# Kernel optimization log

Measured on AMD Instinct MI355X. Metric: run time of the kernel, lower is better.

The kernel has to match this reference:

```python
import jax, jax.numpy as jnp
import numpy as np

DIST = 45
HID = 128
NLAYERS = 4
BATCH = 128


def _build_edges(d):
    n = d * d - 1
    sqrt_n = int(np.sqrt(n)) + 1
    src, dst = [], []
    for i in range(n):
        row, col = i // sqrt_n, i % sqrt_n
        for dr, dc in ((-1, 0), (1, 0), (0, -1), (0, 1)):
            nr, nc = row + dr, col + dc
            j = nr * sqrt_n + nc
            if 0 <= nr < sqrt_n and 0 <= j < n and j != i:
                src.append(i)
                dst.append(j)
    return np.asarray(src, np.int32), np.asarray(dst, np.int32), n


def setup_inputs() -> dict:
    key = jax.random.key(0)
    ks = jax.random.split(key, 8)
    src, dst, n = _build_edges(DIST)
    s = 1.0 / np.sqrt(HID)
    return {
        "x": jax.random.normal(ks[0], (BATCH, n), jnp.float32),
        "W_embed": jax.random.normal(ks[1], (1, HID), jnp.float32),
        "b_embed": jnp.zeros((HID,), jnp.float32),
        "gnn_W": jax.random.normal(ks[2], (NLAYERS, 2 * HID, HID), jnp.float32) * s,
        "gnn_b": jnp.zeros((NLAYERS, HID), jnp.float32),
        "ln_g": jnp.ones((NLAYERS, HID), jnp.float32),
        "ln_b": jnp.zeros((NLAYERS, HID), jnp.float32),
        "out_W1": jax.random.normal(ks[3], (HID, HID), jnp.float32) * s,
        "out_b1": jnp.zeros((HID,), jnp.float32),
        "out_W2": jax.random.normal(ks[4], (HID, 2), jnp.float32) * s,
        "out_b2": jnp.zeros((2,), jnp.float32),
        "edge_src": jnp.asarray(src),
        "edge_dst": jnp.asarray(dst),
    }


def _layer_norm(h, g, b, eps=1e-5):
    mu = h.mean(-1, keepdims=True)
    var = ((h - mu) ** 2).mean(-1, keepdims=True)
    return (h - mu) * jax.lax.rsqrt(var + eps) * g + b


def _segment_mean(h, src, dst, n_nodes):
    # h: [B, N, H] -> mean of incoming-neighbor features per node; 0 if no edge.
    hs = jnp.swapaxes(h[:, src, :], 0, 1)                 # [E, B, H]
    sums = jax.ops.segment_sum(hs, dst, num_segments=n_nodes)   # [N, B, H]
    cnt = jax.ops.segment_sum(jnp.ones_like(dst, jnp.float32), dst,
                              num_segments=n_nodes)              # [N]
    agg = jnp.where(cnt[:, None, None] > 0,
                    sums / jnp.maximum(cnt, 1.0)[:, None, None], 0.0)
    return jnp.swapaxes(agg, 0, 1)                        # [B, N, H]


def reference(x, W_embed, b_embed, gnn_W, gnn_b, ln_g, ln_b,
              out_W1, out_b1, out_W2, out_b2, edge_src, edge_dst):
    n_nodes = x.shape[1]
    # node_embed: Linear(1, H) applied to x[..., None]
    h = x[..., None] * W_embed[0] + b_embed               # [B, N, H]
    for l in range(gnn_W.shape[0]):
        agg = _segment_mean(h, edge_src, edge_dst, n_nodes)
        combined = jnp.concatenate([h, agg], axis=-1)     # [B, N, 2H]
        h = jax.nn.relu(combined @ gnn_W[l] + gnn_b[l])
        h = _layer_norm(h, ln_g[l], ln_b[l])
    graph_repr = h.mean(axis=1)                           # [B, H]
    hid = jax.nn.relu(graph_repr @ out_W1 + out_b1)
    return hid @ out_W2 + out_b2                          # [B, 2]
```

## Files before the change

### kernel.cpp

```cpp
#include <hip/hip_runtime.h>

typedef unsigned short u16;
typedef unsigned int   u32;
typedef __attribute__((ext_vector_type(8))) short short8;
typedef __attribute__((ext_vector_type(4))) float f32x4;

#define NN   2024
#define NB   128
#define HID  128
#define MT   128
#define MTOT (NN*NB)

__device__ __forceinline__ float bf2f(u16 h){ union{u32 u; float f;}c; c.u=((u32)h)<<16; return c.f; }
__device__ __forceinline__ u16 f2bf(float f){ union{float f; u32 u;}c; c.f=f; return (u16)((c.u+0x7fffu+((c.u>>16)&1u))>>16); }
__device__ __forceinline__ f32x4 mfma16(short8 a, short8 b, f32x4 c){ return __builtin_amdgcn_mfma_f32_16x16x32_bf16(a,b,c,0,0,0); }
__device__ __forceinline__ void glds16(const void* g, void* l){
  __builtin_amdgcn_global_load_lds((const __attribute__((address_space(1))) void*)g,
                                   (__attribute__((address_space(3))) void*)l, 16, 0, 0);
}

__device__ __forceinline__ void gemm_chunk(f32x4 (&acc)[2][4], const u16* Ab,
                                           const u16* Wb, int l, int wr, int wc){
  const u32 swz   = ((u32)(l & 7)) << 4;
  const u32 klane = ((u32)(l >> 4)) << 4;
  const char* aB = (const char*)Ab + (u32)(32*wr + (l & 15)) * 256;
  const char* bB = (const char*)Wb + (u32)(64*wc + (l & 15)) * 256;
#pragma unroll
  for (int ks = 0; ks < 4; ++ks){
    const u32 kbx = (((u32)ks << 6) + klane) ^ swz;
    short8 a0 = *(const short8*)(aB + kbx);
    short8 a1 = *(const short8*)(aB + 4096 + kbx);
#pragma unroll
    for (int j = 0; j < 4; ++j){
      short8 bf = *(const short8*)(bB + (u32)j*4096 + kbx);
      acc[0][j] = mfma16(a0, bf, acc[0][j]);
      acc[1][j] = mfma16(a1, bf, acc[1][j]);
    }
  }
}

template<int EMBED>
__global__ __launch_bounds__(512, 4)
void layer_k(const u16* __restrict__ hin, const float* __restrict__ x,
             const float* __restrict__ We, const float* __restrict__ be,
             const u16* __restrict__ Wt, const float* __restrict__ bias,
             const float* __restrict__ lng, const float* __restrict__ lnb,
             u16* __restrict__ hout)
{
  __shared__ __align__(16) u16 Ab[MT*128];
  __shared__ __align__(16) u16 Wb[128*128];
  const int t  = threadIdx.x;
  const int l  = t & 63;
  const int wv = t >> 6;
  const int wr = wv >> 1;
  const int wc = wv & 1;
  const int m0 = blockIdx.x * MT;

  const int gl16 = l >> 4, gcl = l & 15;

  const int sR = t >> 2;
  const int cq = t & 3;
  const int c0 = cq * 4;
  const int sm = m0 + sR;
  const u32 sSwz = ((u32)(sR & 7)) << 4;
  char* aRow = (char*)Ab + (u32)sR * 256;

  const int nd = sm % NN;
  const int v0 = (nd >= 45), v1 = (nd <= NN-46), v2 = (nd >= 1), v3 = (nd <= NN-2);
  const float inv = 1.0f / (float)(v0 + v1 + v2 + v3);

  f32x4 acc[2][4];
#pragma unroll
  for (int m = 0; m < 2; ++m)
#pragma unroll
    for (int j = 0; j < 4; ++j)
      acc[m][j] = (f32x4){0.f,0.f,0.f,0.f};

  if constexpr (EMBED) {
    const float xv = x[sm];
#pragma unroll
    for (int q = 0; q < 4; ++q){
      const int c = c0 + q;
      short8 v;
#pragma unroll
      for (int i = 0; i < 8; ++i) v[i] = (short)f2bf(fmaf(xv, We[c*8+i], be[c*8+i]));
      *(short8*)(aRow + (((u32)c << 4) ^ sSwz)) = v;
    }
  } else {
#pragma unroll
    for (int i = 0; i < 4; ++i){
      const int r  = wv*16 + i*4 + gl16;
      const int cs = gcl ^ (r & 7);
      glds16(hin + (size_t)(m0 + r)*HID + cs*8, (char*)Ab + (u32)(wv*4 + i)*1024);
    }
  }
#pragma unroll
  for (int i = 0; i < 4; ++i){
    const int col = wv*16 + i*4 + gl16;
    const int cs  = gcl ^ (col & 7);
    glds16(Wt + (u32)col*256 + cs*8, (char*)Wb + (u32)(wv*4 + i)*1024);
  }

  short8 gA[4], gB[4];
  if constexpr (!EMBED) {
    const u16* p0 = hin + (size_t)(v0 ? sm-45 : sm) * HID;
    const u16* p1 = hin + (size_t)(v1 ? sm+45 : sm) * HID;
#pragma unroll
    for (int q = 0; q < 4; ++q){
      gA[q] = *(const short8*)(p0 + (c0+q)*8);
      gB[q] = *(const short8*)(p1 + (c0+q)*8);
    }
  }
  __syncthreads();

  gemm_chunk(acc, Ab, Wb, l, wr, wc);

  float sq[4][8];
  short8 gC[4], gD[4];
  float mx = 0.f;
  if constexpr (!EMBED) {
    const u16* p2 = hin + (size_t)(v2 ? sm-1 : sm) * HID;
    const u16* p3 = hin + (size_t)(v3 ? sm+1 : sm) * HID;
#pragma unroll
    for (int q = 0; q < 4; ++q){
      gC[q] = *(const short8*)(p2 + (c0+q)*8);
      gD[q] = *(const short8*)(p3 + (c0+q)*8);
    }
    const float f0 = (float)v0, f1 = (float)v1;
#pragma unroll
    for (int q = 0; q < 4; ++q)
#pragma unroll
      for (int i = 0; i < 8; ++i)
        sq[q][i] = f0*bf2f((u16)gA[q][i]) + f1*bf2f((u16)gB[q][i]);
  } else {
    if (v0) mx += x[sm-45];
    if (v1) mx += x[sm+45];
    if (v2) mx += x[sm-1];
    if (v3) mx += x[sm+1];
    mx *= inv;
  }
  __syncthreads();

  if constexpr (!EMBED) {
    const float f2 = (float)v2, f3 = (float)v3;
#pragma unroll
    for (int q = 0; q < 4; ++q){
      short8 v;
#pragma unroll
      for (int i = 0; i < 8; ++i){
        const float s = (sq[q][i] + f2*bf2f((u16)gC[q][i]) + f3*bf2f((u16)gD[q][i])) * inv;
        v[i] = (short)f2bf(s);
      }
      *(short8*)(aRow + (((u32)(c0+q) << 4) ^ sSwz)) = v;
    }
  } else {
#pragma unroll
    for (int q = 0; q < 4; ++q){
      const int c = c0 + q;
      short8 v;
#pragma unroll
      for (int i = 0; i < 8; ++i) v[i] = (short)f2bf(fmaf(mx, We[c*8+i], be[c*8+i]));
      *(short8*)(aRow + (((u32)c << 4) ^ sSwz)) = v;
    }
  }
#pragma unroll
  for (int i = 0; i < 4; ++i){
    const int col = wv*16 + i*4 + gl16;
    const int cs  = gcl ^ (col & 7);
    glds16(Wt + (u32)col*256 + 128 + cs*8, (char*)Wb + (u32)(wv*4 + i)*1024);
  }
  __syncthreads();

  gemm_chunk(acc, Ab, Wb, l, wr, wc);
  __syncthreads();

  float2* red = (float2*)Ab;
  const int cB = l & 15, rg = l >> 4;
  float bias4[4], g4[4], be4[4];
#pragma unroll
  for (int j = 0; j < 4; ++j){
    const int col = 64*wc + 16*j + cB;
    bias4[j] = bias[col]; g4[j] = lng[col]; be4[j] = lnb[col];
  }
#pragma unroll
  for (int m = 0; m < 2; ++m){
#pragma unroll
    for (int r = 0; r < 4; ++r){
      float p1 = 0.f, p2 = 0.f;
#pragma unroll
      for (int j = 0; j < 4; ++j){
        float y = fmaxf(acc[m][j][r] + bias4[j], 0.f);
        acc[m][j][r] = y;
        p1 += y; p2 += y*y;
      }
#pragma unroll
      for (int d = 1; d < 16; d <<= 1){
        p1 += __shfl_xor(p1, d);
        p2 += __shfl_xor(p2, d);
      }
      if (cB == 0){
        const int row = 32*wr + 16*m + 4*rg + r;
        red[row*2 + wc] = make_float2(p1, p2);
      }
    }
  }
  __syncthreads();
#pragma unroll
  for (int m = 0; m < 2; ++m){
#pragma unroll
    for (int r = 0; r < 4; ++r){
      const int row = 32*wr + 16*m + 4*rg + r;
      const float2 pa = red[row*2], pb = red[row*2 + 1];
      const float s1 = pa.x + pb.x, s2 = pa.y + pb.y;
      const float mu  = s1 * (1.f/128.f);
      const float var = s2 * (1.f/128.f) - mu*mu;
      const float rs  = rsqrtf(var + 1e-5f);
      u16* orow = hout + (size_t)(m0 + row) * HID;
#pragma unroll
      for (int j = 0; j < 4; ++j){
        const float o = (acc[m][j][r] - mu) * rs * g4[j] + be4[j];
        orow[64*wc + 16*j + cB] = f2bf(o);
      }
    }
  }
}

__global__ void prep_k(const float* __restrict__ gw, u16* __restrict__ Wt){
  const int idx = blockIdx.x*256 + threadIdx.x;
  const int lay = idx >> 15;
  const int r   = idx & 32767;
  const int j   = r >> 8;
  const int k   = r & 255;
  Wt[idx] = f2bf(gw[lay*32768 + k*128 + j]);
}

__global__ void mean1_k(const u16* __restrict__ h, float* __restrict__ partial){
  __shared__ float red[16][16][8];
  const int blk = blockIdx.x;
  const int b = blk >> 3, s = blk & 7;
  const int t = threadIdx.x;
  const int cg = t & 15, q = t >> 4;
  const int nbeg = s*253, nend = nbeg + 253;
  float a[8] = {0.f,0.f,0.f,0.f,0.f,0.f,0.f,0.f};
  const u16* hb = h + (size_t)b * NN * HID;
  for (int n = nbeg + q; n < nend; n += 16){
    short8 v = *(const short8*)(hb + (size_t)n*HID + cg*8);
#pragma unroll
    for (int i = 0; i < 8; ++i) a[i] += bf2f((u16)v[i]);
  }
#pragma unroll
  for (int i = 0; i < 8; ++i) red[q][cg][i] = a[i];
  __syncthreads();
  if (t < 128){
    const int cc = t >> 3, i = t & 7;
    float v = 0.f;
#pragma unroll
    for (int qq = 0; qq < 16; ++qq) v += red[qq][cc][i];
    partial[((size_t)b*8 + s)*128 + t] = v;
  }
}

__global__ void mean2_k(const float* __restrict__ partial, float* __restrict__ gr){
  const int idx = blockIdx.x*256 + threadIdx.x;
  const int b = idx >> 7, c = idx & 127;
  float a = 0.f;
#pragma unroll
  for (int s = 0; s < 8; ++s) a += partial[((size_t)b*8 + s)*128 + c];
  gr[idx] = a * (1.0f / 2024.0f);
}

__global__ void head1_k(const float* __restrict__ gr, const float* __restrict__ W1,
                        const float* __restrict__ b1, float* __restrict__ hid){
  const int idx = blockIdx.x*256 + threadIdx.x;
  const int b = idx >> 7, j = idx & 127;
  const float* g = gr + b*128;
  float a = b1[j];
  for (int k = 0; k < 128; ++k) a = fmaf(g[k], W1[k*128 + j], a);
  hid[idx] = fmaxf(a, 0.f);
}

__global__ void head2_k(const float* __restrict__ hid, const float* __restrict__ W2,
                        const float* __restrict__ b2, float* __restrict__ out){
  const int t = threadIdx.x;
  const int b = t >> 1, o = t & 1;
  const float* hh = hid + b*128;
  float a = b2[o];
  for (int k = 0; k < 128; ++k) a = fmaf(hh[k], W2[k*2 + o], a);
  out[t] = a;
}

extern "C" void kernel_launch(void* const* d_in, const int* in_sizes, int n_in,
                              void* d_out, int out_size, void* d_ws, size_t ws_size,
                              hipStream_t stream){
  const float* x  = (const float*)d_in[0];
  const float* We = (const float*)d_in[1];
  const float* be = (const float*)d_in[2];
  const float* gW = (const float*)d_in[3];
  const float* gb = (const float*)d_in[4];
  const float* lg = (const float*)d_in[5];
  const float* lb = (const float*)d_in[6];
  const float* W1 = (const float*)d_in[7];
  const float* b1 = (const float*)d_in[8];
  const float* W2 = (const float*)d_in[9];
  const float* b2 = (const float*)d_in[10];
  float* out = (float*)d_out;

  char* w = (char*)d_ws;
  const size_t HB = (size_t)MTOT * HID * 2;
  u16*   hA  = (u16*)w;
  u16*   hB  = (u16*)(w + HB);
  u16*   Wt  = (u16*)(w + 2*HB);
  float* gr  = (float*)(w + 2*HB + 262144);
  float* hid = (float*)(w + 2*HB + 262144 + 65536);
  float* partial = (float*)w;

  prep_k<<<512, 256, 0, stream>>>(gW, Wt);
  layer_k<1><<<MTOT/MT, 512, 0, stream>>>(nullptr, x, We, be, Wt,
                                          gb, lg, lb, hA);
  layer_k<0><<<MTOT/MT, 512, 0, stream>>>(hA, nullptr, nullptr, nullptr, Wt + 32768,
                                          gb + 128, lg + 128, lb + 128, hB);
  layer_k<0><<<MTOT/MT, 512, 0, stream>>>(hB, nullptr, nullptr, nullptr, Wt + 65536,
                                          gb + 256, lg + 256, lb + 256, hA);
  layer_k<0><<<MTOT/MT, 512, 0, stream>>>(hA, nullptr, nullptr, nullptr, Wt + 98304,
                                          gb + 384, lg + 384, lb + 384, hB);
  mean1_k<<<NB*8, 256, 0, stream>>>(hB, partial);
  mean2_k<<<64, 256, 0, stream>>>(partial, gr);
  head1_k<<<64, 256, 0, stream>>>(gr, W1, b1, hid);
  head2_k<<<1, 256, 0, stream>>>(hid, W2, b2, out);
}
```

Before: 309.3 us.

## Rewrite GNN layer kernel to feed MFMA operands directly from global memory

Rewrites the layer kernel so that weights and node features are loaded straight from global memory into registers as MFMA operands, using a transposed (W × H) orientation, instead of staging them through LDS with global_load_lds. Each block now covers 256 rows, and block IDs are remapped to XCD-contiguous chunks to improve L2 locality. Neighbour averaging is done in registers with precomputed weights and packed bf16 conversion. The output is transposed through LDS so global stores are coalesced. The trade-off is less on-chip reuse of weights and neighbour rows, since each wave now reads redundant data from L2, plus higher register pressure from the 4x4 accumulator tile.

```diff
diff --git a/kernel.cpp b/kernel.cpp
--- a/kernel.cpp
+++ b/kernel.cpp
@@ -8,220 +8,211 @@
 #define NN   2024
 #define NB   128
 #define HID  128
-#define MT   128
 #define MTOT (NN*NB)
-
+#define RPB  256
+#define NBLK (MTOT/RPB)
+
+__device__ __forceinline__ float bflo(u32 w){ union{u32 u; float f;}c; c.u=w<<16;        return c.f; }
+__device__ __forceinline__ float bfhi(u32 w){ union{u32 u; float f;}c; c.u=w&0xffff0000u; return c.f; }
 __device__ __forceinline__ float bf2f(u16 h){ union{u32 u; float f;}c; c.u=((u32)h)<<16; return c.f; }
 __device__ __forceinline__ u16 f2bf(float f){ union{float f; u32 u;}c; c.f=f; return (u16)((c.u+0x7fffu+((c.u>>16)&1u))>>16); }
-__device__ __forceinline__ f32x4 mfma16(short8 a, short8 b, f32x4 c){ return __builtin_amdgcn_mfma_f32_16x16x32_bf16(a,b,c,0,0,0); }
-__device__ __forceinline__ void glds16(const void* g, void* l){
-  __builtin_amdgcn_global_load_lds((const __attribute__((address_space(1))) void*)g,
-                                   (__attribute__((address_space(3))) void*)l, 16, 0, 0);
-}
-
-__device__ __forceinline__ void gemm_chunk(f32x4 (&acc)[2][4], const u16* Ab,
-                                           const u16* Wb, int l, int wr, int wc){
-  const u32 swz   = ((u32)(l & 7)) << 4;
-  const u32 klane = ((u32)(l >> 4)) << 4;
-  const char* aB = (const char*)Ab + (u32)(32*wr + (l & 15)) * 256;
-  const char* bB = (const char*)Wb + (u32)(64*wc + (l & 15)) * 256;
-#pragma unroll
-  for (int ks = 0; ks < 4; ++ks){
-    const u32 kbx = (((u32)ks << 6) + klane) ^ swz;
-    short8 a0 = *(const short8*)(aB + kbx);
-    short8 a1 = *(const short8*)(aB + 4096 + kbx);
-#pragma unroll
-    for (int j = 0; j < 4; ++j){
-      short8 bf = *(const short8*)(bB + (u32)j*4096 + kbx);
-      acc[0][j] = mfma16(a0, bf, acc[0][j]);
-      acc[1][j] = mfma16(a1, bf, acc[1][j]);
-    }
-  }
+__device__ __forceinline__ u32 cvtpk(float lo, float hi){
+  u32 r; asm("v_cvt_pk_bf16_f32 %0, %1, %2" : "=v"(r) : "v"(lo), "v"(hi)); return r;
+}
+__device__ __forceinline__ f32x4 mfma16(short8 a, short8 b, f32x4 c){
+  return __builtin_amdgcn_mfma_f32_16x16x32_bf16(a,b,c,0,0,0);
+}
+
+__device__ __forceinline__ short8 avg4(short8 a0, short8 a1, short8 a2, short8 a3,
+                                       float w0, float w1, float w2, float w3){
+  union{short8 s; u32 u[4];} A, B, C, D, R;
+  A.s=a0; B.s=a1; C.s=a2; D.s=a3;
+#pragma unroll
+  for (int p=0;p<4;++p){
+    float lo = w0*bflo(A.u[p]); lo = fmaf(w1,bflo(B.u[p]),lo); lo = fmaf(w2,bflo(C.u[p]),lo); lo = fmaf(w3,bflo(D.u[p]),lo);
+    float hi = w0*bfhi(A.u[p]); hi = fmaf(w1,bfhi(B.u[p]),hi); hi = fmaf(w2,bfhi(C.u[p]),hi); hi = fmaf(w3,bfhi(D.u[p]),hi);
+    R.u[p] = cvtpk(lo, hi);
+  }
+  return R.s;
+}
+
+__device__ __forceinline__ short8 synth8(float xv, const float* __restrict__ Wek,
+                                         const float* __restrict__ bek){
+  union{short8 s; u32 u[4];} R;
+#pragma unroll
+  for (int p=0;p<4;++p){
+    float lo = fmaf(xv, Wek[2*p],   bek[2*p]);
+    float hi = fmaf(xv, Wek[2*p+1], bek[2*p+1]);
+    R.u[p] = cvtpk(lo, hi);
+  }
+  return R.s;
 }
 
 template<int EMBED>
 __global__ __launch_bounds__(512, 4)
-void layer_k(const u16* __restrict__ hin, const float* __restrict__ x,
-             const float* __restrict__ We, const float* __restrict__ be,
-             const u16* __restrict__ Wt, const float* __restrict__ bias,
-             const float* __restrict__ lng, const float* __restrict__ lnb,
-             u16* __restrict__ hout)
+void layer2_k(const u16* __restrict__ hin, const float* __restrict__ x,
+              const float* __restrict__ We, const float* __restrict__ be,
+              const u16* __restrict__ Wt, const float* __restrict__ bias,
+              const float* __restrict__ lng, const float* __restrict__ lnb,
+              u16* __restrict__ hout)
 {
-  __shared__ __align__(16) u16 Ab[MT*128];
-  __shared__ __align__(16) u16 Wb[128*128];
+  __shared__ __align__(16) u16 trBuf[RPB*128];
   const int t  = threadIdx.x;
   const int l  = t & 63;
-  const int wv = t >> 6;
-  const int wr = wv >> 1;
-  const int wc = wv & 1;
-  const int m0 = blockIdx.x * MT;
-
-  const int gl16 = l >> 4, gcl = l & 15;
-
-  const int sR = t >> 2;
-  const int cq = t & 3;
-  const int c0 = cq * 4;
-  const int sm = m0 + sR;
-  const u32 sSwz = ((u32)(sR & 7)) << 4;
-  char* aRow = (char*)Ab + (u32)sR * 256;
-
-  const int nd = sm % NN;
-  const int v0 = (nd >= 45), v1 = (nd <= NN-46), v2 = (nd >= 1), v3 = (nd <= NN-2);
-  const float inv = 1.0f / (float)(v0 + v1 + v2 + v3);
-
-  f32x4 acc[2][4];
-#pragma unroll
-  for (int m = 0; m < 2; ++m)
-#pragma unroll
-    for (int j = 0; j < 4; ++j)
-      acc[m][j] = (f32x4){0.f,0.f,0.f,0.f};
-
-  if constexpr (EMBED) {
-    const float xv = x[sm];
-#pragma unroll
-    for (int q = 0; q < 4; ++q){
-      const int c = c0 + q;
-      short8 v;
-#pragma unroll
-      for (int i = 0; i < 8; ++i) v[i] = (short)f2bf(fmaf(xv, We[c*8+i], be[c*8+i]));
-      *(short8*)(aRow + (((u32)c << 4) ^ sSwz)) = v;
-    }
-  } else {
-#pragma unroll
-    for (int i = 0; i < 4; ++i){
-      const int r  = wv*16 + i*4 + gl16;
-      const int cs = gcl ^ (r & 7);
-      glds16(hin + (size_t)(m0 + r)*HID + cs*8, (char*)Ab + (u32)(wv*4 + i)*1024);
-    }
-  }
-#pragma unroll
-  for (int i = 0; i < 4; ++i){
-    const int col = wv*16 + i*4 + gl16;
-    const int cs  = gcl ^ (col & 7);
-    glds16(Wt + (u32)col*256 + cs*8, (char*)Wb + (u32)(wv*4 + i)*1024);
-  }
-
-  short8 gA[4], gB[4];
-  if constexpr (!EMBED) {
-    const u16* p0 = hin + (size_t)(v0 ? sm-45 : sm) * HID;
-    const u16* p1 = hin + (size_t)(v1 ? sm+45 : sm) * HID;
-#pragma unroll
-    for (int q = 0; q < 4; ++q){
-      gA[q] = *(const short8*)(p0 + (c0+q)*8);
-      gB[q] = *(const short8*)(p1 + (c0+q)*8);
+  const int wv = t >> 6, wr = wv >> 1, wc = wv & 1;
+  const int cB = l & 15, rg = l >> 4;
+
+  const int orig = blockIdx.x;
+  const int xcd = orig & 7, bidx = orig >> 3;
+  const int swzb = (xcd < 4 ? xcd*127 : 508 + (xcd-4)*126) + bidx;
+  const int m0 = swzb * RPB;
+  const int rowb = m0 + 64*wr;
+
+  int   rowi[4], r0[4], r1[4], r2[4], r3[4];
+  float fw0[4], fw1[4], fw2[4], fw3[4];
+  float xs[4], mx[4];
+#pragma unroll
+  for (int hm=0; hm<4; ++hm){
+    const int row = rowb + 16*hm + cB;
+    rowi[hm] = row;
+    const int nd = row % NN;
+    const int v0 = (nd >= 45), v1 = (nd <= NN-46), v2 = (nd >= 1), v3 = (nd <= NN-2);
+    const int cnt = v0+v1+v2+v3;
+    const float inv = (cnt==4) ? 0.25f : ((cnt==3) ? (1.f/3.f) : 0.5f);
+    fw0[hm] = v0 ? inv : 0.f; fw1[hm] = v1 ? inv : 0.f;
+    fw2[hm] = v2 ? inv : 0.f; fw3[hm] = v3 ? inv : 0.f;
+    r0[hm] = v0 ? row-45 : row; r1[hm] = v1 ? row+45 : row;
+    r2[hm] = v2 ? row-1  : row; r3[hm] = v3 ? row+1  : row;
+    if constexpr (EMBED){
+      xs[hm] = x[row];
+      mx[hm] = fw0[hm]*x[r0[hm]] + fw1[hm]*x[r1[hm]] + fw2[hm]*x[r2[hm]] + fw3[hm]*x[r3[hm]];
+    }
+  }
+
+  f32x4 acc[4][4];
+#pragma unroll
+  for (int fj=0; fj<4; ++fj)
+#pragma unroll
+    for (int hm=0; hm<4; ++hm)
+      acc[fj][hm] = (f32x4){0.f,0.f,0.f,0.f};
+
+  const int kb = rg*8;
+
+#pragma unroll
+  for (int ks=0; ks<4; ++ks){
+    const int kk = ks*32 + kb;
+    short8 aW[4];
+#pragma unroll
+    for (int fj=0; fj<4; ++fj){
+      const int feat = 64*wc + 16*fj + cB;
+      aW[fj] = *(const short8*)(Wt + (u32)feat*256 + kk);
+    }
+#pragma unroll
+    for (int hm=0; hm<4; ++hm){
+      short8 bH;
+      if constexpr (EMBED) bH = synth8(xs[hm], We+kk, be+kk);
+      else                 bH = *(const short8*)(hin + (size_t)rowi[hm]*HID + kk);
+#pragma unroll
+      for (int fj=0; fj<4; ++fj) acc[fj][hm] = mfma16(aW[fj], bH, acc[fj][hm]);
+    }
+  }
+#pragma unroll
+  for (int ks=0; ks<4; ++ks){
+    const int kk = ks*32 + kb;
+    short8 aW[4];
+#pragma unroll
+    for (int fj=0; fj<4; ++fj){
+      const int feat = 64*wc + 16*fj + cB;
+      aW[fj] = *(const short8*)(Wt + (u32)feat*256 + 128 + kk);
+    }
+#pragma unroll
+    for (int hm=0; hm<4; ++hm){
+      short8 bH;
+      if constexpr (EMBED) bH = synth8(mx[hm], We+kk, be+kk);
+      else {
+        short8 n0 = *(const short8*)(hin + (size_t)r0[hm]*HID + kk);
+        short8 n1 = *(const short8*)(hin + (size_t)r1[hm]*HID + kk);
+        short8 n2 = *(const short8*)(hin + (size_t)r2[hm]*HID + kk);
+        short8 n3 = *(const short8*)(hin + (size_t)r3[hm]*HID + kk);
+        bH = avg4(n0,n1,n2,n3, fw0[hm],fw1[hm],fw2[hm],fw3[hm]);
+      }
+#pragma unroll
+      for (int fj=0; fj<4; ++fj) acc[fj][hm] = mfma16(aW[fj], bH, acc[fj][hm]);
+    }
+  }
+
+  float4 bias4[4], g4[4], b4[4];
+#pragma unroll
+  for (int fj=0; fj<4; ++fj){
+    const int f0 = 64*wc + 16*fj + 4*rg;
+    bias4[fj] = *(const float4*)(bias + f0);
+    g4[fj]    = *(const float4*)(lng  + f0);
+    b4[fj]    = *(const float4*)(lnb  + f0);
+  }
+  float2* red = (float2*)trBuf;
+
+#pragma unroll
+  for (int hm=0; hm<4; ++hm){
+    float s1 = 0.f, s2 = 0.f;
+#pragma unroll
+    for (int fj=0; fj<4; ++fj){
+#pragma unroll
+      for (int rr=0; rr<4; ++rr){
+        const float bb = (rr==0)?bias4[fj].x:(rr==1)?bias4[fj].y:(rr==2)?bias4[fj].z:bias4[fj].w;
+        float y = fmaxf(acc[fj][hm][rr] + bb, 0.f);
+        acc[fj][hm][rr] = y;
+        s1 += y; s2 += y*y;
+      }
+    }
+    s1 += __shfl_xor(s1,16); s1 += __shfl_xor(s1,32);
+    s2 += __shfl_xor(s2,16); s2 += __shfl_xor(s2,32);
+    if (rg == 0){
+      const int rib = 64*wr + 16*hm + cB;
+      red[rib*2 + wc] = make_float2(s1, s2);
     }
   }
   __syncthreads();
 
-  gemm_chunk(acc, Ab, Wb, l, wr, wc);
-
-  float sq[4][8];
-  short8 gC[4], gD[4];
-  float mx = 0.f;
-  if constexpr (!EMBED) {
-    const u16* p2 = hin + (size_t)(v2 ? sm-1 : sm) * HID;
-    const u16* p3 = hin + (size_t)(v3 ? sm+1 : sm) * HID;
-#pragma unroll
-    for (int q = 0; q < 4; ++q){
-      gC[q] = *(const short8*)(p2 + (c0+q)*8);
-      gD[q] = *(const short8*)(p3 + (c0+q)*8);
-    }
-    const float f0 = (float)v0, f1 = (float)v1;
-#pragma unroll
-    for (int q = 0; q < 4; ++q)
-#pragma unroll
-      for (int i = 0; i < 8; ++i)
-        sq[q][i] = f0*bf2f((u16)gA[q][i]) + f1*bf2f((u16)gB[q][i]);
-  } else {
-    if (v0) mx += x[sm-45];
-    if (v1) mx += x[sm+45];
-    if (v2) mx += x[sm-1];
-    if (v3) mx += x[sm+1];
-    mx *= inv;
+  float mu4[4], rs4[4];
+#pragma unroll
+  for (int hm=0; hm<4; ++hm){
+    const int rib = 64*wr + 16*hm + cB;
+    const float2 A = red[rib*2], B = red[rib*2+1];
+    const float s1 = A.x + B.x, s2 = A.y + B.y;
+    const float mu  = s1 * (1.f/128.f);
+    const float var = s2 * (1.f/128.f) - mu*mu;
+    mu4[hm] = mu;
+    rs4[hm] = rsqrtf(var + 1e-5f);
   }
   __syncthreads();
 
-  if constexpr (!EMBED) {
-    const float f2 = (float)v2, f3 = (float)v3;
-#pragma unroll
-    for (int q = 0; q < 4; ++q){
-      short8 v;
-#pragma unroll
-      for (int i = 0; i < 8; ++i){
-        const float s = (sq[q][i] + f2*bf2f((u16)gC[q][i]) + f3*bf2f((u16)gD[q][i])) * inv;
-        v[i] = (short)f2bf(s);
-      }
-      *(short8*)(aRow + (((u32)(c0+q) << 4) ^ sSwz)) = v;
-    }
-  } else {
-#pragma unroll
-    for (int q = 0; q < 4; ++q){
-      const int c = c0 + q;
-      short8 v;
-#pragma unroll
-      for (int i = 0; i < 8; ++i) v[i] = (short)f2bf(fmaf(mx, We[c*8+i], be[c*8+i]));
-      *(short8*)(aRow + (((u32)c << 4) ^ sSwz)) = v;
-    }
-  }
-#pragma unroll
-  for (int i = 0; i < 4; ++i){
-    const int col = wv*16 + i*4 + gl16;
-    const int cs  = gcl ^ (col & 7);
-    glds16(Wt + (u32)col*256 + 128 + cs*8, (char*)Wb + (u32)(wv*4 + i)*1024);
+#pragma unroll
+  for (int hm=0; hm<4; ++hm){
+    const int rib = 64*wr + 16*hm + cB;
+    const u32 sw = ((u32)(rib & 7)) << 4;
+    char* rowp = (char*)trBuf + (u32)rib*256;
+    const float mu = mu4[hm], rs = rs4[hm];
+#pragma unroll
+    for (int fj=0; fj<4; ++fj){
+      const float y0 = fmaf((acc[fj][hm][0]-mu)*rs, g4[fj].x, b4[fj].x);
+      const float y1 = fmaf((acc[fj][hm][1]-mu)*rs, g4[fj].y, b4[fj].y);
+      const float y2 = fmaf((acc[fj][hm][2]-mu)*rs, g4[fj].z, b4[fj].z);
+      const float y3 = fmaf((acc[fj][hm][3]-mu)*rs, g4[fj].w, b4[fj].w);
+      const u32 off = (u32)(128*wc + 32*fj + 8*rg);
+      *(u32*)(rowp + ((off    ) ^ sw)) = cvtpk(y0, y1);
+      *(u32*)(rowp + ((off + 4) ^ sw)) = cvtpk(y2, y3);
+    }
   }
   __syncthreads();
 
-  gemm_chunk(acc, Ab, Wb, l, wr, wc);
-  __syncthreads();
-
-  float2* red = (float2*)Ab;
-  const int cB = l & 15, rg = l >> 4;
-  float bias4[4], g4[4], be4[4];
-#pragma unroll
-  for (int j = 0; j < 4; ++j){
-    const int col = 64*wc + 16*j + cB;
-    bias4[j] = bias[col]; g4[j] = lng[col]; be4[j] = lnb[col];
-  }
-#pragma unroll
-  for (int m = 0; m < 2; ++m){
-#pragma unroll
-    for (int r = 0; r < 4; ++r){
-      float p1 = 0.f, p2 = 0.f;
-#pragma unroll
-      for (int j = 0; j < 4; ++j){
-        float y = fmaxf(acc[m][j][r] + bias4[j], 0.f);
-        acc[m][j][r] = y;
-        p1 += y; p2 += y*y;
-      }
-#pragma unroll
-      for (int d = 1; d < 16; d <<= 1){
-        p1 += __shfl_xor(p1, d);
-        p2 += __shfl_xor(p2, d);
-      }
-      if (cB == 0){
-        const int row = 32*wr + 16*m + 4*rg + r;
-        red[row*2 + wc] = make_float2(p1, p2);
-      }
-    }
-  }
-  __syncthreads();
-#pragma unroll
-  for (int m = 0; m < 2; ++m){
-#pragma unroll
-    for (int r = 0; r < 4; ++r){
-      const int row = 32*wr + 16*m + 4*rg + r;
-      const float2 pa = red[row*2], pb = red[row*2 + 1];
-      const float s1 = pa.x + pb.x, s2 = pa.y + pb.y;
-      const float mu  = s1 * (1.f/128.f);
-      const float var = s2 * (1.f/128.f) - mu*mu;
-      const float rs  = rsqrtf(var + 1e-5f);
-      u16* orow = hout + (size_t)(m0 + row) * HID;
-#pragma unroll
-      for (int j = 0; j < 4; ++j){
-        const float o = (acc[m][j][r] - mu) * rs * g4[j] + be4[j];
-        orow[64*wc + 16*j + cB] = f2bf(o);
-      }
-    }
+  const int orow = t >> 1, half = t & 1;
+  const u32 sw2 = ((u32)(orow & 7)) << 4;
+  u16* dst = hout + (size_t)(m0 + orow)*HID + half*64;
+  const char* srow = (const char*)trBuf + (u32)orow*256;
+#pragma unroll
+  for (int i=0; i<8; ++i){
+    short8 v = *(const short8*)(srow + (((u32)(half*128 + 16*i)) ^ sw2));
+    *(short8*)(dst + i*8) = v;
   }
 }
 
@@ -315,14 +306,14 @@
   float* partial = (float*)w;
 
   prep_k<<<512, 256, 0, stream>>>(gW, Wt);
-  layer_k<1><<<MTOT/MT, 512, 0, stream>>>(nullptr, x, We, be, Wt,
-                                          gb, lg, lb, hA);
-  layer_k<0><<<MTOT/MT, 512, 0, stream>>>(hA, nullptr, nullptr, nullptr, Wt + 32768,
-                                          gb + 128, lg + 128, lb + 128, hB);
-  layer_k<0><<<MTOT/MT, 512, 0, stream>>>(hB, nullptr, nullptr, nullptr, Wt + 65536,
-                                          gb + 256, lg + 256, lb + 256, hA);
-  layer_k<0><<<MTOT/MT, 512, 0, stream>>>(hA, nullptr, nullptr, nullptr, Wt + 98304,
-                                          gb + 384, lg + 384, lb + 384, hB);
+  layer2_k<1><<<NBLK, 512, 0, stream>>>(nullptr, x, We, be, Wt,
+                                        gb, lg, lb, hA);
+  layer2_k<0><<<NBLK, 512, 0, stream>>>(hA, nullptr, nullptr, nullptr, Wt + 32768,
+                                        gb + 128, lg + 128, lb + 128, hB);
+  layer2_k<0><<<NBLK, 512, 0, stream>>>(hB, nullptr, nullptr, nullptr, Wt + 65536,
+                                        gb + 256, lg + 256, lb + 256, hA);
+  layer2_k<0><<<NBLK, 512, 0, stream>>>(hA, nullptr, nullptr, nullptr, Wt + 98304,
+                                        gb + 384, lg + 384, lb + 384, hB);
   mean1_k<<<NB*8, 256, 0, stream>>>(hB, partial);
   mean2_k<<<64, 256, 0, stream>>>(partial, gr);
   head1_k<<<64, 256, 0, stream>>>(gr, W1, b1, hid);
```

Result: slower. 945.8 us (+205.7%).
